# Optimization experiments

Hardware: AMD Instinct MI355X
Metric: run time of the kernel (lower is better)

## Reference

```python
import jax, jax.numpy as jnp
import numpy as np

NUM_NODES = 1048576
NUM_FEAT = 128
HIDDEN = 64
NUM_GRAPHS = 4096
OUT_DIM = 5


def setup_inputs() -> dict:
    key = jax.random.key(0)
    ks = jax.random.split(key, 8)
    x = jax.random.normal(ks[0], (NUM_NODES, NUM_FEAT), dtype=jnp.float32)
    batch = jnp.sort(jax.random.randint(ks[1], (NUM_NODES,), 0, NUM_GRAPHS, dtype=jnp.int64))
    s1 = 1.0 / np.sqrt(NUM_FEAT)
    s2 = 1.0 / np.sqrt(HIDDEN)
    W1 = jax.random.uniform(ks[2], (NUM_FEAT, HIDDEN), jnp.float32, -s1, s1)
    b1 = jax.random.uniform(ks[3], (HIDDEN,), jnp.float32, -s1, s1)
    W2 = jax.random.uniform(ks[4], (HIDDEN, HIDDEN), jnp.float32, -s2, s2)
    b2 = jax.random.uniform(ks[5], (HIDDEN,), jnp.float32, -s2, s2)
    W3 = jax.random.uniform(ks[6], (HIDDEN, OUT_DIM), jnp.float32, -s2, s2)
    b3 = jax.random.uniform(ks[7], (OUT_DIM,), jnp.float32, -s2, s2)
    return {"x": x, "batch": batch, "W1": W1, "b1": b1, "W2": W2, "b2": b2, "W3": W3, "b3": b3}


def reference(x, batch, W1, b1, W2, b2, W3, b3):
    # Segment-mean pooling over nodes -> [NUM_GRAPHS, NUM_FEAT]
    sums = jax.ops.segment_sum(x, batch, num_segments=NUM_GRAPHS)
    counts = jax.ops.segment_sum(jnp.ones((x.shape[0],), x.dtype), batch, num_segments=NUM_GRAPHS)
    pooled = jnp.where(counts[:, None] > 0, sums / jnp.maximum(counts, 1.0)[:, None], jnp.zeros((), x.dtype))
    # MLP head: feat -> hidden -> hidden -> 5
    h = jax.nn.relu(pooled @ W1 + b1)
    h = jax.nn.relu(h @ W2 + b2)
    return h @ W3 + b3
```

## Files before the change

### kernel.cpp

```cpp
#include <hip/hip_runtime.h>

#define NUM_NODES  1048576
#define NUM_FEAT   128
#define HIDDEN     64
#define NUM_GRAPHS 4096
#define OUT_DIM    5

typedef float f32x4 __attribute__((ext_vector_type(4)));

__global__ __launch_bounds__(128, 8) void pool_kernel(
    const float* __restrict__ x,
    const int*   __restrict__ batch,
    float* __restrict__ pooled)
{
    const int g = blockIdx.x;
    const int t = threadIdx.x;
    const int lane = t & 63;
    const int T = g + (t >> 6);

    int lo = 0, hi = NUM_NODES;
    while (hi - lo > 64) {
        const int w = hi - lo;
        const int base = lo;
        const int pos = base + (int)(((long long)w * lane) >> 6);
        const unsigned long long bal = __ballot(batch[pos] < T);
        const int m = __popcll(bal);
        if (m == 0) {
            hi = lo;
        } else {
            lo = base + (int)(((long long)w * (m - 1)) >> 6) + 1;
            if (m < 64) hi = base + (int)(((long long)w * m) >> 6);
        }
    }
    if (hi > lo) {
        const int w = hi - lo;
        const bool pred = (lane < w) ? (batch[lo + lane] < T) : false;
        lo += __popcll(__ballot(pred));
    }

    __shared__ int bounds[2];
    if (lane == 0) bounds[t >> 6] = lo;
    __syncthreads();
    const int start = bounds[0];
    const int end   = bounds[1];
    const int count = end - start;

    const int cg = t & 31;
    const int ro = t >> 5;
    int iters = count - ro + 3;
    iters = (iters > 0) ? (iters >> 2) : 0;

    const f32x4* p = reinterpret_cast<const f32x4*>(
        x + (size_t)(start + ro) * NUM_FEAT) + cg;
    const int step = NUM_FEAT;

    f32x4 acc0 = (f32x4)0.0f, acc1 = (f32x4)0.0f;
    int i = 0;
    for (; i + 2 <= iters; i += 2) {
        const f32x4 v0 = __builtin_nontemporal_load(p);
        const f32x4 v1 = __builtin_nontemporal_load(p + step);
        acc0 += v0;
        acc1 += v1;
        p += 2 * step;
    }
    if (i < iters) acc0 += __builtin_nontemporal_load(p);

    __shared__ f32x4 part[128];
    part[t] = acc0 + acc1;
    __syncthreads();

    if (t < 32) {
        f32x4 s = part[t] + part[t + 32] + part[t + 64] + part[t + 96];
        const float inv = (count > 0) ? (1.0f / (float)count) : 0.0f;
        s *= inv;
        *(reinterpret_cast<f32x4*>(pooled + (size_t)g * NUM_FEAT) + t) = s;
    }
}

__global__ __launch_bounds__(256) void mlp_kernel(
    const float* __restrict__ pooled,
    const float* __restrict__ W1, const float* __restrict__ b1,
    const float* __restrict__ W2, const float* __restrict__ b2,
    const float* __restrict__ W3, const float* __restrict__ b3,
    float* __restrict__ out)
{
    __shared__ float W1s[NUM_FEAT * HIDDEN];
    __shared__ float W2s[HIDDEN * HIDDEN];
    __shared__ float W3s[HIDDEN * OUT_DIM];
    __shared__ float b1s[HIDDEN], b2s[HIDDEN], b3s[OUT_DIM];
    __shared__ float pr[4][NUM_FEAT];
    __shared__ float h1s[4][HIDDEN], h2s[4][HIDDEN];

    const int t = threadIdx.x;

    for (int i = t; i < NUM_FEAT * HIDDEN / 4; i += 256)
        ((f32x4*)W1s)[i] = ((const f32x4*)W1)[i];
    for (int i = t; i < HIDDEN * HIDDEN / 4; i += 256)
        ((f32x4*)W2s)[i] = ((const f32x4*)W2)[i];
    for (int i = t; i < HIDDEN * OUT_DIM; i += 256)
        W3s[i] = W3[i];
    if (t < HIDDEN) { b1s[t] = b1[t]; b2s[t] = b2[t]; }
    if (t < OUT_DIM) b3s[t] = b3[t];
    __syncthreads();

    const int gbase = blockIdx.x * 16;
    for (int it = 0; it < 4; ++it) {
        const int g0 = gbase + it * 4;

        if (t < 128) {
            const int row = t >> 5, e = t & 31;
            ((f32x4*)pr[row])[e] =
                *(reinterpret_cast<const f32x4*>(pooled + (size_t)(g0 + row) * NUM_FEAT) + e);
        }
        __syncthreads();

        const int q = t >> 6, h = t & 63;
        float s = b1s[h];
        #pragma unroll 8
        for (int k = 0; k < NUM_FEAT; ++k) s = fmaf(pr[q][k], W1s[k * HIDDEN + h], s);
        h1s[q][h] = fmaxf(s, 0.0f);
        __syncthreads();

        s = b2s[h];
        #pragma unroll 8
        for (int k = 0; k < HIDDEN; ++k) s = fmaf(h1s[q][k], W2s[k * HIDDEN + h], s);
        h2s[q][h] = fmaxf(s, 0.0f);
        __syncthreads();

        if (t < 4 * OUT_DIM) {
            const int qq = t / OUT_DIM, o = t % OUT_DIM;
            float so = b3s[o];
            #pragma unroll 8
            for (int k = 0; k < HIDDEN; ++k) so = fmaf(h2s[qq][k], W3s[k * OUT_DIM + o], so);
            out[(size_t)(g0 + qq) * OUT_DIM + o] = so;
        }
        __syncthreads();
    }
}

extern "C" void kernel_launch(void* const* d_in, const int* in_sizes, int n_in,
                              void* d_out, int out_size, void* d_ws, size_t ws_size,
                              hipStream_t stream) {
    const float* x     = (const float*)d_in[0];
    const int*   batch = (const int*)d_in[1];
    const float* W1    = (const float*)d_in[2];
    const float* b1    = (const float*)d_in[3];
    const float* W2    = (const float*)d_in[4];
    const float* b2    = (const float*)d_in[5];
    const float* W3    = (const float*)d_in[6];
    const float* b3    = (const float*)d_in[7];
    float* out = (float*)d_out;

    float* pooled = (float*)d_ws;

    pool_kernel<<<NUM_GRAPHS, 128, 0, stream>>>(x, batch, pooled);
    mlp_kernel<<<NUM_GRAPHS / 16, 256, 0, stream>>>(pooled, W1, b1, W2, b2, W3, b3, out);
}
```

Measured before the change: 109.8 us.

## Precompute segment offsets in a boundary-scan kernel and double MLP grid size

New measurement: 105.9 us. -3.6%, faster.

```diff
diff --git a/kernel.cpp b/kernel.cpp
--- a/kernel.cpp
+++ b/kernel.cpp
@@ -8,45 +8,34 @@
 
 typedef float f32x4 __attribute__((ext_vector_type(4)));
 
+__global__ __launch_bounds__(256) void seg_scan_kernel(
+    const int* __restrict__ batch, int* __restrict__ seg)
+{
+    const int i = blockIdx.x * blockDim.x + threadIdx.x;
+    if (i >= NUM_NODES) return;
+    const int b = batch[i];
+    const int prev = (i == 0) ? -1 : batch[i - 1];
+    for (int g = prev + 1; g <= b; ++g) seg[g] = i;
+    if (i == NUM_NODES - 1) {
+        for (int g = b + 1; g <= NUM_GRAPHS; ++g) seg[g] = NUM_NODES;
+    }
+}
+
 __global__ __launch_bounds__(128, 8) void pool_kernel(
     const float* __restrict__ x,
-    const int*   __restrict__ batch,
+    const int*   __restrict__ seg,
     float* __restrict__ pooled)
 {
     const int g = blockIdx.x;
     const int t = threadIdx.x;
-    const int lane = t & 63;
-    const int T = g + (t >> 6);
 
-    int lo = 0, hi = NUM_NODES;
-    while (hi - lo > 64) {
-        const int w = hi - lo;
-        const int base = lo;
-        const int pos = base + (int)(((long long)w * lane) >> 6);
-        const unsigned long long bal = __ballot(batch[pos] < T);
-        const int m = __popcll(bal);
-        if (m == 0) {
-            hi = lo;
-        } else {
-            lo = base + (int)(((long long)w * (m - 1)) >> 6) + 1;
-            if (m < 64) hi = base + (int)(((long long)w * m) >> 6);
-        }
-    }
-    if (hi > lo) {
-        const int w = hi - lo;
-        const bool pred = (lane < w) ? (batch[lo + lane] < T) : false;
-        lo += __popcll(__ballot(pred));
-    }
-
-    __shared__ int bounds[2];
-    if (lane == 0) bounds[t >> 6] = lo;
-    __syncthreads();
-    const int start = bounds[0];
-    const int end   = bounds[1];
+    const int start = seg[g];
+    const int end   = seg[g + 1];
     const int count = end - start;
 
     const int cg = t & 31;
     const int ro = t >> 5;
+
     int iters = count - ro + 3;
     iters = (iters > 0) ? (iters >> 2) : 0;
 
@@ -103,8 +92,8 @@
     if (t < OUT_DIM) b3s[t] = b3[t];
     __syncthreads();
 
-    const int gbase = blockIdx.x * 16;
-    for (int it = 0; it < 4; ++it) {
+    const int gbase = blockIdx.x * 8;
+    for (int it = 0; it < 2; ++it) {
         const int g0 = gbase + it * 4;
 
         if (t < 128) {
@@ -151,8 +140,10 @@
     const float* b3    = (const float*)d_in[7];
     float* out = (float*)d_out;
 
-    float* pooled = (float*)d_ws;
+    int*   seg    = (int*)d_ws;
+    float* pooled = (float*)((char*)d_ws + 32768);
 
-    pool_kernel<<<NUM_GRAPHS, 128, 0, stream>>>(x, batch, pooled);
-    mlp_kernel<<<NUM_GRAPHS / 16, 256, 0, stream>>>(pooled, W1, b1, W2, b2, W3, b3, out);
+    seg_scan_kernel<<<NUM_NODES / 256, 256, 0, stream>>>(batch, seg);
+    pool_kernel<<<NUM_GRAPHS, 128, 0, stream>>>(x, seg, pooled);
+    mlp_kernel<<<NUM_GRAPHS / 8, 256, 0, stream>>>(pooled, W1, b1, W2, b2, W3, b3, out);
 }
```
